# Kernel optimization log

Measured on AMD Instinct MI355X. Metric: run time of the kernel, lower is better.

The kernel has to match this reference:

```python
import jax, jax.numpy as jnp
import numpy as np

D_IN = 768
D_OUT = 768
NUM_HEADS = 12
HEAD_DIM = D_OUT // NUM_HEADS


def setup_inputs() -> dict:
    key = jax.random.key(0)
    ks = jax.random.split(key, 6)
    s = 0.02
    x = jax.random.normal(ks[0], (4, 1024, D_IN), dtype=jnp.float32)
    # torch Linear weights are [out_features, in_features]
    Wq = jax.random.normal(ks[1], (D_OUT, D_IN), dtype=jnp.float32) * s
    Wk = jax.random.normal(ks[2], (D_OUT, D_IN), dtype=jnp.float32) * s
    Wv = jax.random.normal(ks[3], (D_OUT, D_IN), dtype=jnp.float32) * s
    Wo = jax.random.normal(ks[4], (D_OUT, D_OUT), dtype=jnp.float32) * s
    bo = jax.random.normal(ks[5], (D_OUT,), dtype=jnp.float32) * s
    return {"x": x, "Wq": Wq, "Wk": Wk, "Wv": Wv, "Wo": Wo, "bo": bo}


def reference(x, Wq, Wk, Wv, Wo, bo):
    B, T, _ = x.shape
    H, Dh = NUM_HEADS, HEAD_DIM
    # QKV projections (no bias), reshape to [B, H, T, Dh]
    q = (x @ Wq.T).reshape(B, T, H, Dh).transpose(0, 2, 1, 3)
    k = (x @ Wk.T).reshape(B, T, H, Dh).transpose(0, 2, 1, 3)
    v = (x @ Wv.T).reshape(B, T, H, Dh).transpose(0, 2, 1, 3)
    # Scores [B, H, T, T]. NOTE: original torch code's masked_fill and dropout
    # are not in-place / not assigned, so neither affects the output.
    scores = jnp.einsum("bhqd,bhkd->bhqk", q, k)
    attn = jax.nn.softmax(scores / np.sqrt(Dh).astype(np.float32), axis=-1)
    ctx = jnp.einsum("bhqk,bhkd->bhqd", attn, v)
    ctx = ctx.transpose(0, 2, 1, 3).reshape(B, T, H * Dh)
    return ctx @ Wo.T + bo
```

## Files before the change

kernel.cpp:

```cpp
#include <hip/hip_runtime.h>

typedef _Float16 half8 __attribute__((ext_vector_type(8)));
typedef float f32x4 __attribute__((ext_vector_type(4)));
typedef unsigned short u16;

#define NHEAD 12
#define DHEAD 64
#define DM    768
#define TSEQ  1024
#define LOG2E 1.44269504f

static constexpr size_t OFF_XH  = 0;
static constexpr size_t OFF_WQH = 3145728;
static constexpr size_t OFF_WKH = 3735552;
static constexpr size_t OFF_WVH = 4325376;
static constexpr size_t OFF_WOH = 4915200;
static constexpr size_t OFF_Q   = 5505024;
static constexpr size_t OFF_K   = 8650752;
static constexpr size_t OFF_VT  = 11796480;
static constexpr size_t OFF_CTX = 0;
static constexpr size_t OFF_OP  = 14942208;
static constexpr size_t OFF_ML_BYTES = 42467328;
static constexpr size_t WS_NEED_SPLITK = 43253760;

typedef const __attribute__((address_space(1))) void* gas_ptr;
typedef __attribute__((address_space(3))) void* las_ptr;
__device__ __forceinline__ void gload16(const _Float16* g, _Float16* l) {
    __builtin_amdgcn_global_load_lds((gas_ptr)g, (las_ptr)l, 16, 0, 0);
}

template <int CTRL>
__device__ __forceinline__ float dpp_rotf(float x) {
    int r = __builtin_amdgcn_update_dpp(0, __builtin_bit_cast(int, x), CTRL, 0xF, 0xF, true);
    return __builtin_bit_cast(float, r);
}
__device__ __forceinline__ float row16_max(float x) {
    x = fmaxf(x, dpp_rotf<0x121>(x));
    x = fmaxf(x, dpp_rotf<0x122>(x));
    x = fmaxf(x, dpp_rotf<0x124>(x));
    x = fmaxf(x, dpp_rotf<0x128>(x));
    return x;
}
__device__ __forceinline__ float row16_add(float x) {
    x = x + dpp_rotf<0x121>(x);
    x = x + dpp_rotf<0x122>(x);
    x = x + dpp_rotf<0x124>(x);
    x = x + dpp_rotf<0x128>(x);
    return x;
}

__global__ void cvt_kernel(const float* __restrict__ x, const float* __restrict__ wq,
                           const float* __restrict__ wk, const float* __restrict__ wv,
                           const float* __restrict__ wo, _Float16* __restrict__ ws) {
    int seg = blockIdx.y;
    const float* src;
    _Float16* dst;
    int n;
    if (seg == 0)      { src = x;  dst = ws + OFF_XH;  n = 3145728; }
    else if (seg == 1) { src = wq; dst = ws + OFF_WQH; n = 589824; }
    else if (seg == 2) { src = wk; dst = ws + OFF_WKH; n = 589824; }
    else if (seg == 3) { src = wv; dst = ws + OFF_WVH; n = 589824; }
    else               { src = wo; dst = ws + OFF_WOH; n = 589824; }
    int i = (blockIdx.x * blockDim.x + threadIdx.x) * 8;
    if (i < n) {
        float4 v0 = *(const float4*)(src + i);
        float4 v1 = *(const float4*)(src + i + 4);
        half8 o;
        o[0] = (_Float16)v0.x; o[1] = (_Float16)v0.y;
        o[2] = (_Float16)v0.z; o[3] = (_Float16)v0.w;
        o[4] = (_Float16)v1.x; o[5] = (_Float16)v1.y;
        o[6] = (_Float16)v1.z; o[7] = (_Float16)v1.w;
        *(half8*)(dst + i) = o;
    }
}

__global__ __launch_bounds__(256) void qkv_kernel(_Float16* __restrict__ ws) {
    __shared__ __align__(16) _Float16 ldsA[128 * 32];
    __shared__ __align__(16) _Float16 ldsB[128 * 32];

    const int z = blockIdx.z;
    const _Float16* __restrict__ xh = ws + OFF_XH;
    const _Float16* __restrict__ w  = ws + (z == 0 ? OFF_WQH : z == 1 ? OFF_WKH : OFF_WVH);
    _Float16* __restrict__ outp     = ws + (z == 0 ? OFF_Q   : z == 1 ? OFF_K   : OFF_VT);

    const int tid  = threadIdx.x;
    const int lane = tid & 63;
    const int wid  = tid >> 6;
    const int quad = lane >> 4, l15 = lane & 15;
    const int wm = (wid & 1) * 64, wn = (wid >> 1) * 64;

    int mb, nb;
    const _Float16 *gA, *gB;
    if (z < 2) {
        mb = blockIdx.x * 128;
        nb = blockIdx.y * 128;
        gA = xh + (size_t)mb * DM;
        gB = w  + (size_t)nb * DM;
    } else {
        mb = blockIdx.y * 128;
        nb = blockIdx.x * 128;
        gA = w  + (size_t)mb * DM;
        gB = xh + (size_t)nb * DM;
    }

    const int srow = (lane >> 2);
    const int scol = (lane & 3) * 8;
    const size_t goff0 = (size_t)(wid * 32 + srow) * DM + scol;
    const size_t goff1 = (size_t)(wid * 32 + 16 + srow) * DM + scol;
    _Float16* lA0 = ldsA + wid * 1024;
    _Float16* lA1 = ldsA + wid * 1024 + 512;
    _Float16* lB0 = ldsB + wid * 1024;
    _Float16* lB1 = ldsB + wid * 1024 + 512;

    f32x4 acc[4][4] = {};
    for (int k0 = 0; k0 < DM; k0 += 32) {
        gload16(gA + goff0 + k0, lA0);
        gload16(gA + goff1 + k0, lA1);
        gload16(gB + goff0 + k0, lB0);
        gload16(gB + goff1 + k0, lB1);
        __syncthreads();

        half8 a[4], b[4];
#pragma unroll
        for (int t = 0; t < 4; t++) {
            a[t] = *(const half8*)(ldsA + (wm + t * 16 + l15) * 32 + quad * 8);
            b[t] = *(const half8*)(ldsB + (wn + t * 16 + l15) * 32 + quad * 8);
        }
#pragma unroll
        for (int mt = 0; mt < 4; mt++)
#pragma unroll
            for (int nt = 0; nt < 4; nt++)
                acc[mt][nt] = __builtin_amdgcn_mfma_f32_16x16x32_f16(a[mt], b[nt], acc[mt][nt], 0, 0, 0);
        __syncthreads();
    }

#pragma unroll
    for (int mt = 0; mt < 4; mt++)
#pragma unroll
        for (int nt = 0; nt < 4; nt++)
#pragma unroll
            for (int r = 0; r < 4; r++) {
                int m = mb + wm + mt * 16 + quad * 4 + r;
                int n = nb + wn + nt * 16 + l15;
                size_t idx;
                if (z < 2) {
                    int bb = m >> 10, tt = m & 1023;
                    int h = n >> 6, d = n & 63;
                    idx = ((size_t)(bb * NHEAD + h) * TSEQ + tt) * DHEAD + d;
                } else {
                    int h = m >> 6, d = m & 63;
                    int bb = n >> 10, tt = n & 1023;
                    idx = ((size_t)(bb * NHEAD + h) * DHEAD + d) * TSEQ + tt;
                }
                outp[idx] = (_Float16)acc[mt][nt][r];
            }
}

template <int NZ>
__device__ __forceinline__ void attn_body(_Float16* __restrict__ ws) {
    __shared__ __align__(16) _Float16 ldsK[64 * 64];
    __shared__ __align__(16) _Float16 ldsV[64 * 64];
    __shared__ __align__(16) _Float16 ldsP[4][16 * 72];

    const int tid  = threadIdx.x;
    const int lane = tid & 63;
    const int wid  = tid >> 6;
    const int quad = lane >> 4, l15 = lane & 15;
    const int bh = blockIdx.y;
    const int z  = (NZ > 1) ? blockIdx.z : 0;
    const int q0 = blockIdx.x * 64 + wid * 16;
    const int kbeg = z * (TSEQ / NZ), kend = kbeg + TSEQ / NZ;

    const _Float16* __restrict__ Q  = ws + OFF_Q  + (size_t)bh * TSEQ * DHEAD;
    const _Float16* __restrict__ K  = ws + OFF_K  + (size_t)bh * TSEQ * DHEAD;
    const _Float16* __restrict__ VT = ws + OFF_VT + (size_t)bh * DHEAD * TSEQ;
    _Float16* pbase = ldsP[wid];

    const int srow0 = tid >> 3, sc0 = tid & 7;
    const int ldsOff0 = srow0 * 64 + ((sc0 ^ (srow0 & 7)) * 8);
    const int ldsOff1 = (srow0 + 32) * 64 + ((sc0 ^ (srow0 & 7)) * 8);

    half8 qf[2];
#pragma unroll
    for (int ks = 0; ks < 2; ks++) {
        qf[ks] = *(const half8*)(Q + (size_t)(q0 + l15) * DHEAD + ks * 32 + quad * 8);
        qf[ks] = qf[ks] * (_Float16)0.125f;
    }

    float mrun[4], lrun[4];
    f32x4 oacc[4] = {};
#pragma unroll
    for (int r = 0; r < 4; r++) { mrun[r] = -1e30f; lrun[r] = 0.f; }

    uint4 ka, kb, va, vb;
    ka = *(const uint4*)(K + kbeg * DHEAD + tid * 8);
    kb = *(const uint4*)(K + kbeg * DHEAD + 2048 + tid * 8);
    va = *(const uint4*)(VT + (size_t)srow0 * TSEQ + kbeg + sc0 * 8);
    vb = *(const uint4*)(VT + (size_t)(srow0 + 32) * TSEQ + kbeg + sc0 * 8);

    for (int kt = kbeg; kt < kend; kt += 64) {
        *(uint4*)(ldsK + ldsOff0) = ka;
        *(uint4*)(ldsK + ldsOff1) = kb;
        *(uint4*)(ldsV + ldsOff0) = va;
        *(uint4*)(ldsV + ldsOff1) = vb;
        __syncthreads();

        if (kt + 64 < kend) {
            ka = *(const uint4*)(K + (kt + 64) * DHEAD + tid * 8);
            kb = *(const uint4*)(K + (kt + 64) * DHEAD + 2048 + tid * 8);
            va = *(const uint4*)(VT + (size_t)srow0 * TSEQ + kt + 64 + sc0 * 8);
            vb = *(const uint4*)(VT + (size_t)(srow0 + 32) * TSEQ + kt + 64 + sc0 * 8);
        }

        half8 kf[4][2];
#pragma unroll
        for (int n = 0; n < 4; n++)
#pragma unroll
            for (int ks = 0; ks < 2; ks++) {
                int row = n * 16 + l15;
                int phys = (ks * 4 + quad) ^ (row & 7);
                kf[n][ks] = *(const half8*)(ldsK + row * 64 + phys * 8);
            }

        f32x4 s[4] = {};
#pragma unroll
        for (int n = 0; n < 4; n++)
#pragma unroll
            for (int ks = 0; ks < 2; ks++)
                s[n] = __builtin_amdgcn_mfma_f32_16x16x32_f16(qf[ks], kf[n][ks], s[n], 0, 0, 0);

#pragma unroll
        for (int r = 0; r < 4; r++) {
            float tm = fmaxf(fmaxf(s[0][r], s[1][r]), fmaxf(s[2][r], s[3][r]));
            tm = row16_max(tm);
            float mnew = fmaxf(mrun[r], tm);
            float alpha = __builtin_amdgcn_exp2f((mrun[r] - mnew) * LOG2E);
            mrun[r] = mnew;
            float mL = mnew * LOG2E;
            float ts = 0.f;
#pragma unroll
            for (int n = 0; n < 4; n++) {
                float e = __builtin_amdgcn_exp2f(__builtin_fmaf(s[n][r], LOG2E, -mL));
                s[n][r] = e;
                ts += e;
            }
            ts = row16_add(ts);
            lrun[r] = __builtin_fmaf(lrun[r], alpha, ts);
#pragma unroll
            for (int dn = 0; dn < 4; dn++) oacc[dn][r] *= alpha;
        }

#pragma unroll
        for (int n = 0; n < 4; n++)
#pragma unroll
            for (int r = 0; r < 4; r++)
                pbase[(quad * 4 + r) * 72 + n * 16 + l15] = (_Float16)s[n][r];

        half8 vf[4][2];
#pragma unroll
        for (int dn = 0; dn < 4; dn++)
#pragma unroll
            for (int ks = 0; ks < 2; ks++) {
                int row = dn * 16 + l15;
                int phys = (ks * 4 + quad) ^ (row & 7);
                vf[dn][ks] = *(const half8*)(ldsV + row * 64 + phys * 8);
            }

        half8 pf[2];
#pragma unroll
        for (int ks = 0; ks < 2; ks++)
            pf[ks] = *(const half8*)(pbase + l15 * 72 + ks * 32 + quad * 8);

#pragma unroll
        for (int dn = 0; dn < 4; dn++)
#pragma unroll
            for (int ks = 0; ks < 2; ks++)
                oacc[dn] = __builtin_amdgcn_mfma_f32_16x16x32_f16(pf[ks], vf[dn][ks], oacc[dn], 0, 0, 0);

        __syncthreads();
    }

    if (NZ == 1) {
        _Float16* __restrict__ ctx = ws + OFF_CTX;
        const int b_ = bh / NHEAD, h = bh % NHEAD;
#pragma unroll
        for (int dn = 0; dn < 4; dn++)
#pragma unroll
            for (int r = 0; r < 4; r++) {
                int t_ = q0 + quad * 4 + r;
                int col = h * DHEAD + dn * 16 + l15;
                float v = oacc[dn][r] / lrun[r];
                ctx[((size_t)(b_ * TSEQ + t_)) * DM + col] = (_Float16)v;
            }
    } else {
        _Float16* __restrict__ op = ws + OFF_OP;
        float* __restrict__ ml = (float*)((char*)ws + OFF_ML_BYTES);
        const size_t rowbase = (size_t)z * 48 * TSEQ + (size_t)bh * TSEQ + q0;
#pragma unroll
        for (int dn = 0; dn < 4; dn++)
#pragma unroll
            for (int r = 0; r < 4; r++) {
                size_t row = rowbase + quad * 4 + r;
                op[row * 64 + dn * 16 + l15] = (_Float16)oacc[dn][r];
            }
        if (l15 == 0) {
#pragma unroll
            for (int r = 0; r < 4; r++) {
                size_t row = rowbase + quad * 4 + r;
                ml[row * 2]     = mrun[r];
                ml[row * 2 + 1] = lrun[r];
            }
        }
    }
}

__global__ __launch_bounds__(256, 3) void attn_kernel(_Float16* __restrict__ ws) {
    attn_body<1>(ws);
}
__global__ __launch_bounds__(256, 4) void attn_splitk_kernel(_Float16* __restrict__ ws) {
    attn_body<2>(ws);
}

__global__ __launch_bounds__(256) void combine_kernel(_Float16* __restrict__ ws) {
    const _Float16* __restrict__ op = ws + OFF_OP;
    const float* __restrict__ ml = (const float*)((const char*)ws + OFF_ML_BYTES);
    _Float16* __restrict__ ctx = ws + OFF_CTX;

    int g = blockIdx.x * 256 + threadIdx.x;
    int row = g >> 3, chunk = g & 7;
    int bh = row >> 10, q = row & 1023;
    int b_ = bh / NHEAD, h = bh % NHEAD;

    float m0 = ml[(size_t)row * 2], l0 = ml[(size_t)row * 2 + 1];
    float m1 = ml[(size_t)(49152 + row) * 2], l1 = ml[(size_t)(49152 + row) * 2 + 1];
    float M = fmaxf(m0, m1);
    float w0 = __builtin_amdgcn_exp2f((m0 - M) * LOG2E);
    float w1 = __builtin_amdgcn_exp2f((m1 - M) * LOG2E);
    float inv_l = 1.0f / (w0 * l0 + w1 * l1);

    half8 o0 = *(const half8*)(op + (size_t)row * 64 + chunk * 8);
    half8 o1 = *(const half8*)(op + (size_t)(49152 + row) * 64 + chunk * 8);
    half8 o;
#pragma unroll
    for (int j = 0; j < 8; j++)
        o[j] = (_Float16)(((float)o0[j] * w0 + (float)o1[j] * w1) * inv_l);
    *(half8*)(ctx + ((size_t)(b_ * TSEQ + q)) * DM + h * DHEAD + chunk * 8) = o;
}

__global__ __launch_bounds__(256) void proj_kernel(const _Float16* __restrict__ ws,
                                                   const float* __restrict__ bo,
                                                   float* __restrict__ out) {
    __shared__ __align__(16) _Float16 ldsA[64 * 32];
    __shared__ __align__(16) _Float16 ldsB[64 * 32];

    const _Float16* __restrict__ gA = ws + OFF_CTX + (size_t)blockIdx.x * 64 * DM;
    const _Float16* __restrict__ gB = ws + OFF_WOH + (size_t)blockIdx.y * 64 * DM;

    const int tid  = threadIdx.x;
    const int lane = tid & 63;
    const int wid  = tid >> 6;
    const int quad = lane >> 4, l15 = lane & 15;
    const int wm = (wid & 1) * 32, wn = (wid >> 1) * 32;

    const int srow = tid >> 2;
    const int scol = (tid & 3) * 8;
    const size_t goff = (size_t)srow * DM + scol;
    _Float16* lA = ldsA + wid * 512;
    _Float16* lB = ldsB + wid * 512;

    f32x4 acc[2][2] = {};
    for (int k0 = 0; k0 < DM; k0 += 32) {
        gload16(gA + goff + k0, lA);
        gload16(gB + goff + k0, lB);
        __syncthreads();

        half8 a[2], b[2];
#pragma unroll
        for (int t = 0; t < 2; t++) {
            a[t] = *(const half8*)(ldsA + (wm + t * 16 + l15) * 32 + quad * 8);
            b[t] = *(const half8*)(ldsB + (wn + t * 16 + l15) * 32 + quad * 8);
        }
#pragma unroll
        for (int mt = 0; mt < 2; mt++)
#pragma unroll
            for (int nt = 0; nt < 2; nt++)
                acc[mt][nt] = __builtin_amdgcn_mfma_f32_16x16x32_f16(a[mt], b[nt], acc[mt][nt], 0, 0, 0);
        __syncthreads();
    }

    const int mb = blockIdx.x * 64, nb = blockIdx.y * 64;
#pragma unroll
    for (int mt = 0; mt < 2; mt++)
#pragma unroll
        for (int nt = 0; nt < 2; nt++)
#pragma unroll
            for (int r = 0; r < 4; r++) {
                int m = mb + wm + mt * 16 + quad * 4 + r;
                int n = nb + wn + nt * 16 + l15;
                out[(size_t)m * DM + n] = acc[mt][nt][r] + bo[n];
            }
}

extern "C" void kernel_launch(void* const* d_in, const int* in_sizes, int n_in,
                              void* d_out, int out_size, void* d_ws, size_t ws_size,
                              hipStream_t stream) {
    const float* x  = (const float*)d_in[0];
    const float* wq = (const float*)d_in[1];
    const float* wk = (const float*)d_in[2];
    const float* wv = (const float*)d_in[3];
    const float* wo = (const float*)d_in[4];
    const float* bo = (const float*)d_in[5];
    _Float16* ws = (_Float16*)d_ws;
    float* out = (float*)d_out;

    cvt_kernel<<<dim3(1536, 5, 1), 256, 0, stream>>>(x, wq, wk, wv, wo, ws);
    qkv_kernel<<<dim3(32, 6, 3), 256, 0, stream>>>(ws);
    if (ws_size >= WS_NEED_SPLITK) {
        attn_splitk_kernel<<<dim3(16, 48, 2), 256, 0, stream>>>(ws);
        combine_kernel<<<dim3(1536, 1, 1), 256, 0, stream>>>(ws);
    } else {
        attn_kernel<<<dim3(16, 48, 1), 256, 0, stream>>>(ws);
    }
    proj_kernel<<<dim3(64, 12, 1), 256, 0, stream>>>(ws, bo, out);
}
```

Before: 156.5 us.

## Double GEMM K-tile, lazy softmax rescale, and flatten conversion grid

The QKV and output-projection GEMMs now stage a 64-wide K slice per iteration instead of 32, halving the number of barrier pairs and loop trips at the cost of twice the LDS footprint. The attention inner loop skips the running-max update and the rescaling of the accumulator and row sum unless some row's new max exceeds the stored one by more than 4 in any lane, which saves exp and multiply work but lets unnormalized values grow up to e^4 in fp16/fp32. The conversion kernel now uses one flat grid over the contiguous workspace segments instead of a 5-row grid with idle tail blocks.

```diff
diff --git a/kernel.cpp b/kernel.cpp
--- a/kernel.cpp
+++ b/kernel.cpp
@@ -52,31 +52,26 @@
 __global__ void cvt_kernel(const float* __restrict__ x, const float* __restrict__ wq,
                            const float* __restrict__ wk, const float* __restrict__ wv,
                            const float* __restrict__ wo, _Float16* __restrict__ ws) {
-    int seg = blockIdx.y;
+    int i = (blockIdx.x * 256 + threadIdx.x) * 8;
     const float* src;
-    _Float16* dst;
-    int n;
-    if (seg == 0)      { src = x;  dst = ws + OFF_XH;  n = 3145728; }
-    else if (seg == 1) { src = wq; dst = ws + OFF_WQH; n = 589824; }
-    else if (seg == 2) { src = wk; dst = ws + OFF_WKH; n = 589824; }
-    else if (seg == 3) { src = wv; dst = ws + OFF_WVH; n = 589824; }
-    else               { src = wo; dst = ws + OFF_WOH; n = 589824; }
-    int i = (blockIdx.x * blockDim.x + threadIdx.x) * 8;
-    if (i < n) {
-        float4 v0 = *(const float4*)(src + i);
-        float4 v1 = *(const float4*)(src + i + 4);
-        half8 o;
-        o[0] = (_Float16)v0.x; o[1] = (_Float16)v0.y;
-        o[2] = (_Float16)v0.z; o[3] = (_Float16)v0.w;
-        o[4] = (_Float16)v1.x; o[5] = (_Float16)v1.y;
-        o[6] = (_Float16)v1.z; o[7] = (_Float16)v1.w;
-        *(half8*)(dst + i) = o;
-    }
+    if (i < 3145728)      src = x  + i;
+    else if (i < 3735552) src = wq + (i - 3145728);
+    else if (i < 4325376) src = wk + (i - 3735552);
+    else if (i < 4915200) src = wv + (i - 4325376);
+    else                  src = wo + (i - 4915200);
+    float4 v0 = *(const float4*)(src);
+    float4 v1 = *(const float4*)(src + 4);
+    half8 o;
+    o[0] = (_Float16)v0.x; o[1] = (_Float16)v0.y;
+    o[2] = (_Float16)v0.z; o[3] = (_Float16)v0.w;
+    o[4] = (_Float16)v1.x; o[5] = (_Float16)v1.y;
+    o[6] = (_Float16)v1.z; o[7] = (_Float16)v1.w;
+    *(half8*)(ws + i) = o;
 }
 
 __global__ __launch_bounds__(256) void qkv_kernel(_Float16* __restrict__ ws) {
-    __shared__ __align__(16) _Float16 ldsA[128 * 32];
-    __shared__ __align__(16) _Float16 ldsB[128 * 32];
+    __shared__ __align__(16) _Float16 ldsA[128 * 64];
+    __shared__ __align__(16) _Float16 ldsB[128 * 64];
 
     const int z = blockIdx.z;
     const _Float16* __restrict__ xh = ws + OFF_XH;
@@ -103,34 +98,32 @@
         gB = xh + (size_t)nb * DM;
     }
 
-    const int srow = (lane >> 2);
-    const int scol = (lane & 3) * 8;
-    const size_t goff0 = (size_t)(wid * 32 + srow) * DM + scol;
-    const size_t goff1 = (size_t)(wid * 32 + 16 + srow) * DM + scol;
-    _Float16* lA0 = ldsA + wid * 1024;
-    _Float16* lA1 = ldsA + wid * 1024 + 512;
-    _Float16* lB0 = ldsB + wid * 1024;
-    _Float16* lB1 = ldsB + wid * 1024 + 512;
+    const int srow = tid >> 3;
+    const int scol = (tid & 7) * 8;
 
     f32x4 acc[4][4] = {};
-    for (int k0 = 0; k0 < DM; k0 += 32) {
-        gload16(gA + goff0 + k0, lA0);
-        gload16(gA + goff1 + k0, lA1);
-        gload16(gB + goff0 + k0, lB0);
-        gload16(gB + goff1 + k0, lB1);
-        __syncthreads();
-
-        half8 a[4], b[4];
-#pragma unroll
-        for (int t = 0; t < 4; t++) {
-            a[t] = *(const half8*)(ldsA + (wm + t * 16 + l15) * 32 + quad * 8);
-            b[t] = *(const half8*)(ldsB + (wn + t * 16 + l15) * 32 + quad * 8);
-        }
-#pragma unroll
-        for (int mt = 0; mt < 4; mt++)
-#pragma unroll
-            for (int nt = 0; nt < 4; nt++)
-                acc[mt][nt] = __builtin_amdgcn_mfma_f32_16x16x32_f16(a[mt], b[nt], acc[mt][nt], 0, 0, 0);
+    for (int k0 = 0; k0 < DM; k0 += 64) {
+#pragma unroll
+        for (int c = 0; c < 4; c++) {
+            gload16(gA + (size_t)(c * 32 + srow) * DM + scol + k0, ldsA + c * 2048 + wid * 512);
+            gload16(gB + (size_t)(c * 32 + srow) * DM + scol + k0, ldsB + c * 2048 + wid * 512);
+        }
+        __syncthreads();
+
+#pragma unroll
+        for (int ks = 0; ks < 2; ks++) {
+            half8 a[4], b[4];
+#pragma unroll
+            for (int t = 0; t < 4; t++) {
+                a[t] = *(const half8*)(ldsA + (wm + t * 16 + l15) * 64 + ks * 32 + quad * 8);
+                b[t] = *(const half8*)(ldsB + (wn + t * 16 + l15) * 64 + ks * 32 + quad * 8);
+            }
+#pragma unroll
+            for (int mt = 0; mt < 4; mt++)
+#pragma unroll
+                for (int nt = 0; nt < 4; nt++)
+                    acc[mt][nt] = __builtin_amdgcn_mfma_f32_16x16x32_f16(a[mt], b[nt], acc[mt][nt], 0, 0, 0);
+        }
         __syncthreads();
     }
 
@@ -229,14 +222,28 @@
             for (int ks = 0; ks < 2; ks++)
                 s[n] = __builtin_amdgcn_mfma_f32_16x16x32_f16(qf[ks], kf[n][ks], s[n], 0, 0, 0);
 
+        float tm[4];
 #pragma unroll
         for (int r = 0; r < 4; r++) {
-            float tm = fmaxf(fmaxf(s[0][r], s[1][r]), fmaxf(s[2][r], s[3][r]));
-            tm = row16_max(tm);
-            float mnew = fmaxf(mrun[r], tm);
-            float alpha = __builtin_amdgcn_exp2f((mrun[r] - mnew) * LOG2E);
-            mrun[r] = mnew;
-            float mL = mnew * LOG2E;
+            float t = fmaxf(fmaxf(s[0][r], s[1][r]), fmaxf(s[2][r], s[3][r]));
+            tm[r] = row16_max(t);
+        }
+        float need = fmaxf(fmaxf(tm[0] - mrun[0], tm[1] - mrun[1]),
+                           fmaxf(tm[2] - mrun[2], tm[3] - mrun[3]));
+        if (!__all(need <= 4.0f)) {
+#pragma unroll
+            for (int r = 0; r < 4; r++) {
+                float mnew = fmaxf(mrun[r], tm[r]);
+                float alpha = __builtin_amdgcn_exp2f((mrun[r] - mnew) * LOG2E);
+                mrun[r] = mnew;
+                lrun[r] *= alpha;
+#pragma unroll
+                for (int dn = 0; dn < 4; dn++) oacc[dn][r] *= alpha;
+            }
+        }
+#pragma unroll
+        for (int r = 0; r < 4; r++) {
+            float mL = mrun[r] * LOG2E;
             float ts = 0.f;
 #pragma unroll
             for (int n = 0; n < 4; n++) {
@@ -245,9 +252,7 @@
                 ts += e;
             }
             ts = row16_add(ts);
-            lrun[r] = __builtin_fmaf(lrun[r], alpha, ts);
-#pragma unroll
-            for (int dn = 0; dn < 4; dn++) oacc[dn][r] *= alpha;
+            lrun[r] += ts;
         }
 
 #pragma unroll
@@ -350,8 +355,8 @@
 __global__ __launch_bounds__(256) void proj_kernel(const _Float16* __restrict__ ws,
                                                    const float* __restrict__ bo,
                                                    float* __restrict__ out) {
-    __shared__ __align__(16) _Float16 ldsA[64 * 32];
-    __shared__ __align__(16) _Float16 ldsB[64 * 32];
+    __shared__ __align__(16) _Float16 ldsA[64 * 64];
+    __shared__ __align__(16) _Float16 ldsB[64 * 64];
 
     const _Float16* __restrict__ gA = ws + OFF_CTX + (size_t)blockIdx.x * 64 * DM;
     const _Float16* __restrict__ gB = ws + OFF_WOH + (size_t)blockIdx.y * 64 * DM;
@@ -362,29 +367,32 @@
     const int quad = lane >> 4, l15 = lane & 15;
     const int wm = (wid & 1) * 32, wn = (wid >> 1) * 32;
 
-    const int srow = tid >> 2;
-    const int scol = (tid & 3) * 8;
-    const size_t goff = (size_t)srow * DM + scol;
-    _Float16* lA = ldsA + wid * 512;
-    _Float16* lB = ldsB + wid * 512;
+    const int srow = tid >> 3;
+    const int scol = (tid & 7) * 8;
 
     f32x4 acc[2][2] = {};
-    for (int k0 = 0; k0 < DM; k0 += 32) {
-        gload16(gA + goff + k0, lA);
-        gload16(gB + goff + k0, lB);
-        __syncthreads();
-
-        half8 a[2], b[2];
-#pragma unroll
-        for (int t = 0; t < 2; t++) {
-            a[t] = *(const half8*)(ldsA + (wm + t * 16 + l15) * 32 + quad * 8);
-            b[t] = *(const half8*)(ldsB + (wn + t * 16 + l15) * 32 + quad * 8);
-        }
-#pragma unroll
-        for (int mt = 0; mt < 2; mt++)
-#pragma unroll
-            for (int nt = 0; nt < 2; nt++)
-                acc[mt][nt] = __builtin_amdgcn_mfma_f32_16x16x32_f16(a[mt], b[nt], acc[mt][nt], 0, 0, 0);
+    for (int k0 = 0; k0 < DM; k0 += 64) {
+#pragma unroll
+        for (int c = 0; c < 2; c++) {
+            gload16(gA + (size_t)(c * 32 + srow) * DM + scol + k0, ldsA + c * 2048 + wid * 512);
+            gload16(gB + (size_t)(c * 32 + srow) * DM + scol + k0, ldsB + c * 2048 + wid * 512);
+        }
+        __syncthreads();
+
+#pragma unroll
+        for (int ks = 0; ks < 2; ks++) {
+            half8 a[2], b[2];
+#pragma unroll
+            for (int t = 0; t < 2; t++) {
+                a[t] = *(const half8*)(ldsA + (wm + t * 16 + l15) * 64 + ks * 32 + quad * 8);
+                b[t] = *(const half8*)(ldsB + (wn + t * 16 + l15) * 64 + ks * 32 + quad * 8);
+            }
+#pragma unroll
+            for (int mt = 0; mt < 2; mt++)
+#pragma unroll
+                for (int nt = 0; nt < 2; nt++)
+                    acc[mt][nt] = __builtin_amdgcn_mfma_f32_16x16x32_f16(a[mt], b[nt], acc[mt][nt], 0, 0, 0);
+        }
         __syncthreads();
     }
 
@@ -413,7 +421,7 @@
     _Float16* ws = (_Float16*)d_ws;
     float* out = (float*)d_out;
 
-    cvt_kernel<<<dim3(1536, 5, 1), 256, 0, stream>>>(x, wq, wk, wv, wo, ws);
+    cvt_kernel<<<dim3(2688, 1, 1), 256, 0, stream>>>(x, wq, wk, wv, wo, ws);
     qkv_kernel<<<dim3(32, 6, 3), 256, 0, stream>>>(ws);
     if (ws_size >= WS_NEED_SPLITK) {
         attn_splitk_kernel<<<dim3(16, 48, 2), 256, 0, stream>>>(ws);
```

Result: slower. 162.2 us (+3.6%).
